# Optimization experiments

Measured on AMD Instinct MI355X. Metric: run time of the kernel, lower is better.

## Reference

```python
import jax, jax.numpy as jnp
import numpy as np

B, N, F_IN, HID, HEADS, LAYERS = 512, 128, 128, 64, 4, 3
NEG_SLOPE = 0.2  # DenseGATConv default


def setup_inputs() -> dict:
    key = jax.random.key(0)
    ks = jax.random.split(key, 1 + 4 * LAYERS)
    inp = {}
    inp["x"] = jax.random.normal(ks[0], (B * N, F_IN), jnp.float32)
    # uniform graph sizes: graph i owns nodes [i*N, (i+1)*N)
    inp["batch_mask"] = jnp.repeat(jnp.arange(B, dtype=jnp.int32), N)
    dims = [F_IN] + [HID * HEADS] * (LAYERS - 1)
    for l in range(LAYERS):
        d = dims[l]
        k = 4 * l
        inp[f"W{l}"] = jax.random.normal(ks[1 + k], (d, HEADS * HID), jnp.float32) / np.sqrt(d)
        inp[f"att_src{l}"] = jax.random.normal(ks[2 + k], (HEADS, HID), jnp.float32) * 0.1
        inp[f"att_dst{l}"] = jax.random.normal(ks[3 + k], (HEADS, HID), jnp.float32) * 0.1
        inp[f"b{l}"] = jnp.zeros((HEADS * HID,), jnp.float32)  # zero-init bias, as in PyG
    return inp


def _dense_gat(x, adj, W, att_src, att_dst, bias):
    # x: [B, N, F_in], adj: [N, N] (shared structure, broadcast over batch)
    b, n, _ = x.shape
    h = (x @ W).reshape(b, n, HEADS, HID)                       # [B,N,H,C]
    a_src = jnp.einsum('bnhc,hc->bnh', h, att_src)              # [B,N,H]
    a_dst = jnp.einsum('bnhc,hc->bnh', h, att_dst)              # [B,N,H]
    # alpha[b,i,j,h] = a_src[b,j,h] + a_dst[b,i,h]
    alpha = a_src[:, None, :, :] + a_dst[:, :, None, :]         # [B,N,N,H]
    alpha = jnp.where(alpha >= 0, alpha, NEG_SLOPE * alpha)
    alpha = jnp.where(adj[None, :, :, None] == 0, -jnp.inf, alpha)
    alpha = jax.nn.softmax(alpha, axis=2)                       # softmax over sources j
    out = jnp.einsum('bijh,bjhc->bihc', alpha, h)               # [B,N,H,C]
    return out.reshape(b, n, HEADS * HID) + bias                # concat heads + bias


def reference(x, batch_mask, W0, att_src0, att_dst0, b0,
              W1, att_src1, att_dst1, b1, W2, att_src2, att_dst2, b2):
    # to_dense_batch with uniform graph sizes == reshape; batch_mask encodes this layout
    h = x.reshape(B, N, F_IN)
    eye = jnp.eye(N, dtype=x.dtype)
    # GNNBlock builds full adjacency with zeroed diagonal ...
    adj = jnp.ones((N, N), x.dtype) - eye
    # ... and DenseGATConv(add_loop=True) re-adds self-loops
    adj = jnp.maximum(adj, eye)
    params = [(W0, att_src0, att_dst0, b0), (W1, att_src1, att_dst1, b1),
              (W2, att_src2, att_dst2, b2)]
    for (W, a_s, a_d, b) in params:
        h = _dense_gat(h, adj, W, a_s, a_d, b)
        # block act is nn.LeakyReLU(True): negative_slope=True==1.0 -> identity
        h = jnp.where(h >= 0, h, 1.0 * h)
    return h.sum(axis=1)  # [B, HEADS*HID]
```

## Files before the change

kernel.cpp:

```cpp
#include <hip/hip_runtime.h>
#include <hip/hip_bf16.h>


typedef unsigned short u16;
typedef __attribute__((ext_vector_type(8))) short short8;
typedef __attribute__((ext_vector_type(4))) float f32x4;

#define L2E 1.44269504088896340736f

__device__ __forceinline__ u16 f2bf(float f) {
  unsigned int u = __float_as_uint(f);
  u += 0x7fffu + ((u >> 16) & 1u);
  return (u16)(u >> 16);
}
__device__ __forceinline__ unsigned int pk2(float a, float b) {
  __hip_bfloat162 h2 = __float22bfloat162_rn(make_float2(a, b));
  unsigned int u;
  __builtin_memcpy(&u, &h2, 4);
  return u;
}

__device__ __forceinline__ int xs_byte(int row, int col) {
  return (row << 9) + ((col << 1) ^ ((row & 7) << 4));
}
__device__ __forceinline__ int ht_byte(int row, int col) {
  return (row << 8) + ((col << 1) ^ ((row & 7) << 4));
}

__global__ void prep_w(const float* __restrict__ W0, const float* __restrict__ W1,
                       const float* __restrict__ W2,
                       const float* __restrict__ as0, const float* __restrict__ ad0,
                       const float* __restrict__ as1, const float* __restrict__ ad1,
                       const float* __restrict__ as2, const float* __restrict__ ad2,
                       u16* __restrict__ wt) {
  const int bid = blockIdx.x, tid = threadIdx.x;
  if (bid < 80) {
    const float* W; int NKB, base, rel;
    if (bid < 16)      { W = W0; NKB = 4; base = 0;      rel = bid; }
    else if (bid < 48) { W = W1; NKB = 8; base = 34816;  rel = bid - 16; }
    else               { W = W2; NKB = 8; base = 104448; rel = bid - 48; }
    const int kb = rel >> 2, ko = rel & 3;
    const int n = tid;
    union { u16 v[8]; short8 s; } u;
    #pragma unroll
    for (int e = 0; e < 8; ++e)
      u.v[e] = f2bf(W[(kb * 32 + ko * 8 + e) * 256 + n]);
    const int t = n >> 4, l15 = n & 15;
    *(short8*)(wt + base + (((t * NKB + kb) * 64 + l15 + (ko << 4)) << 3)) = u.s;
  } else if (bid < 100) {
    int b2 = bid - 80;
    const float* W; const float* as; const float* ad; int NKB, base, kb;
    if (b2 < 4)       { W = W0; as = as0; ad = ad0; NKB = 4; base = 0;      kb = b2; }
    else if (b2 < 12) { W = W1; as = as1; ad = ad1; NKB = 8; base = 34816;  kb = b2 - 4; }
    else              { W = W2; as = as2; ad = ad2; NKB = 8; base = 104448; kb = b2 - 12; }
    const int kloc = tid >> 3, col = tid & 7, h = col & 3;
    const int k = kb * 32 + kloc;
    const float* av = (col < 4) ? as : ad;
    float acc = 0.f;
    #pragma unroll 8
    for (int c = 0; c < 64; ++c)
      acc = fmaf(W[k * 256 + h * 64 + c], av[h * 64 + c], acc);
    const int lane2 = col + ((kloc >> 3) << 4), e = kloc & 7;
    const int tb = base + ((16 * NKB + kb) << 9);
    wt[tb + ((lane2) << 3) + e]     = f2bf(acc);
    wt[tb + ((lane2 + 8) << 3) + e] = 0;
  }
}

__global__ __launch_bounds__(512, 4) void gat_all(
    const float* __restrict__ x, const u16* __restrict__ wt,
    const float* __restrict__ bb0, const float* __restrict__ bb1,
    const float* __restrict__ bb2, float* __restrict__ out)
{
  constexpr int AB = 0;
  constexpr int SB = 65536;
  constexpr int DB = 67584;
  constexpr int PM = 69632;
  constexpr int BS = 69696;
  constexpr int OA = 70720;
  __shared__ __align__(16) unsigned char smem[71744];

  float* sbuf  = (float*)(smem + SB);
  float* dbuf  = (float*)(smem + DB);
  float* pmaxw = (float*)(smem + PM);
  float* bsb   = (float*)(smem + BS);
  float* oac   = (float*)(smem + OA);

  const int b    = blockIdx.x;
  const int tid  = threadIdx.x;
  const int w    = tid >> 6;
  const int lane = tid & 63;
  const int l15  = lane & 15;
  const int lg   = lane >> 4;

  {
    const float4* xg = (const float4*)(x + (size_t)b * (128 * 128));
    #pragma unroll
    for (int it = 0; it < 8; ++it) {
      int e = tid + it * 512;
      float4 v = xg[e];
      int row = e >> 5, c = (e & 31) << 2;
      uint2 u = { pk2(v.x, v.y), pk2(v.z, v.w) };
      *(uint2*)(smem + AB + xs_byte(row, c)) = u;
    }
  }
  __syncthreads();

  const u16* wfl[3]    = {wt, wt + 34816, wt + 104448};
  const float* bias[3] = {bb0, bb1, bb2};

  #pragma unroll
  for (int l = 0; l < 3; ++l) {
    const int NKB = (l == 0) ? 4 : 8;
    const u16* wf = wfl[l];

    if (tid < 256) {
      bsb[tid] = bias[l][tid];
      if (l == 2) oac[tid] = 0.f;
    }

    const int mw = w & 1, nw = w >> 1;
    f32x4 acc[4][4] = {};
    for (int ks = 0; ks < NKB; ++ks) {
      const int kcol = ks * 32 + lg * 8;
      short8 afr[4];
      #pragma unroll
      for (int mi = 0; mi < 4; ++mi)
        afr[mi] = *(const short8*)(smem + AB + xs_byte(mw * 64 + mi * 16 + l15, kcol));
      #pragma unroll
      for (int nh = 0; nh < 2; ++nh) {
        short8 bfr[2];
        #pragma unroll
        for (int ni2 = 0; ni2 < 2; ++ni2) {
          int t = nw * 4 + nh * 2 + ni2;
          bfr[ni2] = *(const short8*)(wf + (((t * NKB + ks) * 64 + lane) << 3));
        }
        #pragma unroll
        for (int mi = 0; mi < 4; ++mi)
          #pragma unroll
          for (int ni2 = 0; ni2 < 2; ++ni2)
            acc[mi][nh * 2 + ni2] = __builtin_amdgcn_mfma_f32_16x16x32_bf16(
                afr[mi], bfr[ni2], acc[mi][nh * 2 + ni2], 0, 0, 0);
      }
    }

    if (w >= 4) {
      const int mw2 = w & 1, mih = (w >> 1) & 1;
      f32x4 acc2[2] = {};
      for (int ks = 0; ks < NKB; ++ks) {
        const int kcol = ks * 32 + lg * 8;
        short8 bsd = *(const short8*)(wf + (((16 * NKB + ks) * 64 + lane) << 3));
        #pragma unroll
        for (int mi2 = 0; mi2 < 2; ++mi2) {
          short8 a = *(const short8*)(smem + AB +
              xs_byte(mw2 * 64 + (mih * 2 + mi2) * 16 + l15, kcol));
          acc2[mi2] = __builtin_amdgcn_mfma_f32_16x16x32_bf16(a, bsd, acc2[mi2], 0, 0, 0);
        }
      }
      float mx = -3.4e38f;
      #pragma unroll
      for (int mi2 = 0; mi2 < 2; ++mi2) {
        f32x4 v = acc2[mi2] * L2E;
        if (l15 < 8) {
          float* basep = (float*)(smem + (l15 < 4 ? SB : DB))
                       + (l15 & 3) * 128 + mw2 * 64 + (mih * 2 + mi2) * 16 + lg * 4;
          *(float4*)basep = (float4){v[0], v[1], v[2], v[3]};
        }
        mx = fmaxf(mx, fmaxf(fmaxf(v[0], v[1]), fmaxf(v[2], v[3])));
      }
      mx = fmaxf(mx, __shfl_xor(mx, 16));
      mx = fmaxf(mx, __shfl_xor(mx, 32));
      if (lane < 4) pmaxw[lane * 4 + (w - 4)] = mx;
    }
    __syncthreads();

    #pragma unroll
    for (int mi = 0; mi < 4; ++mi) {
      int j0 = mw * 64 + mi * 16 + lg * 4;
      #pragma unroll
      for (int ni = 0; ni < 4; ++ni) {
        int c = nw * 64 + ni * 16 + l15;
        uint2 u = { pk2(acc[mi][ni][0], acc[mi][ni][1]),
                    pk2(acc[mi][ni][2], acc[mi][ni][3]) };
        *(uint2*)(smem + AB + ht_byte(c, j0)) = u;
      }
    }
    __syncthreads();

    {
      const int hw = w >> 1, ih = w & 1;
      f32x4 facc[4][4] = {};
      float den[4] = {0.f, 0.f, 0.f, 0.f};
      float dvv[4], nml[4];
      const float smax = fmaxf(fmaxf(pmaxw[hw * 4], pmaxw[hw * 4 + 1]),
                               fmaxf(pmaxw[hw * 4 + 2], pmaxw[hw * 4 + 3]));
      #pragma unroll
      for (int ni = 0; ni < 4; ++ni) {
        int i = ih * 64 + ni * 16 + l15;
        dvv[ni] = dbuf[hw * 128 + i];
        float tm = smax + dvv[ni];
        nml[ni] = -fmaxf(tm, 0.2f * tm);
      }
      #pragma unroll
      for (int ks = 0; ks < 4; ++ks) {
        const int j0 = ks * 32 + lg * 8;
        float4 s03 = *(const float4*)(sbuf + hw * 128 + j0);
        float4 s47 = *(const float4*)(sbuf + hw * 128 + j0 + 4);
        float sj[8] = {s03.x, s03.y, s03.z, s03.w, s47.x, s47.y, s47.z, s47.w};
        short8 afr[4];
        #pragma unroll
        for (int mi = 0; mi < 4; ++mi)
          afr[mi] = *(const short8*)(smem + AB + ht_byte(hw * 64 + mi * 16 + l15, j0));
        #pragma unroll
        for (int ni = 0; ni < 4; ++ni) {
          union { short8 s; unsigned int u[4]; } pk;
          float dsum = 0.f;
          #pragma unroll
          for (int t2 = 0; t2 < 4; ++t2) {
            float ta = sj[2 * t2] + dvv[ni];
            ta = fmaxf(ta, 0.2f * ta);
            float ea = exp2f(ta + nml[ni]);
            float tb = sj[2 * t2 + 1] + dvv[ni];
            tb = fmaxf(tb, 0.2f * tb);
            float eb = exp2f(tb + nml[ni]);
            dsum += ea + eb;
            pk.u[t2] = pk2(ea, eb);
          }
          den[ni] += dsum;
          #pragma unroll
          for (int mi = 0; mi < 4; ++mi)
            facc[mi][ni] = __builtin_amdgcn_mfma_f32_16x16x32_bf16(
                afr[mi], pk.s, facc[mi][ni], 0, 0, 0);
        }
      }
      float rvv[4];
      #pragma unroll
      for (int ni = 0; ni < 4; ++ni) {
        float d2 = den[ni];
        d2 += __shfl_xor(d2, 16);
        d2 += __shfl_xor(d2, 32);
        rvv[ni] = 1.f / d2;
      }
      __syncthreads();

      if (l < 2) {
        #pragma unroll
        for (int mi = 0; mi < 4; ++mi) {
          int c0 = hw * 64 + mi * 16 + lg * 4;
          float b0v = bsb[c0], b1v = bsb[c0 + 1], b2v = bsb[c0 + 2], b3v = bsb[c0 + 3];
          #pragma unroll
          for (int ni = 0; ni < 4; ++ni) {
            int i = ih * 64 + ni * 16 + l15;
            float r = rvv[ni];
            uint2 u = { pk2(fmaf(facc[mi][ni][0], r, b0v), fmaf(facc[mi][ni][1], r, b1v)),
                        pk2(fmaf(facc[mi][ni][2], r, b2v), fmaf(facc[mi][ni][3], r, b3v)) };
            *(uint2*)(smem + AB + xs_byte(i, c0)) = u;
          }
        }
      } else {
        #pragma unroll
        for (int mi = 0; mi < 4; ++mi) {
          #pragma unroll
          for (int reg = 0; reg < 4; ++reg) {
            float pv2 = facc[mi][0][reg] * rvv[0] + facc[mi][1][reg] * rvv[1]
                      + facc[mi][2][reg] * rvv[2] + facc[mi][3][reg] * rvv[3];
            pv2 += __shfl_xor(pv2, 1);
            pv2 += __shfl_xor(pv2, 2);
            pv2 += __shfl_xor(pv2, 4);
            pv2 += __shfl_xor(pv2, 8);
            if (l15 == 0)
              atomicAdd(&oac[hw * 64 + mi * 16 + lg * 4 + reg], pv2);
          }
        }
      }
    }
    __syncthreads();
  }

  if (tid < 256) out[(size_t)b * 256 + tid] = oac[tid] + 128.f * bsb[tid];
}

extern "C" void kernel_launch(void* const* d_in, const int* in_sizes, int n_in,
                              void* d_out, int out_size, void* d_ws, size_t ws_size,
                              hipStream_t stream) {
  const float* x   = (const float*)d_in[0];
  const float* W0  = (const float*)d_in[2];
  const float* as0 = (const float*)d_in[3];
  const float* ad0 = (const float*)d_in[4];
  const float* b0  = (const float*)d_in[5];
  const float* W1  = (const float*)d_in[6];
  const float* as1 = (const float*)d_in[7];
  const float* ad1 = (const float*)d_in[8];
  const float* b1  = (const float*)d_in[9];
  const float* W2  = (const float*)d_in[10];
  const float* as2 = (const float*)d_in[11];
  const float* ad2 = (const float*)d_in[12];
  const float* b2  = (const float*)d_in[13];
  u16* wt = (u16*)d_ws;

  hipLaunchKernelGGL(prep_w, dim3(100), dim3(256), 0, stream,
                     W0, W1, W2, as0, ad0, as1, ad1, as2, ad2, wt);
  hipLaunchKernelGGL(gat_all, dim3(512), dim3(512), 0, stream,
                     x, wt, b0, b1, b2, (float*)d_out);
}
```

Before: 186.5 us.

## Split projection and aggregation into two passes with packed bf16 register staging

The feature projection GEMM and the attention aggregation now each run in two column or row halves. Results are packed to bf16 in registers right after each half, which lowers the peak live fp32 accumulator count. The attention-score GEMM is spread over all 8 waves instead of 4, so the per-wave max reduction buffer grows to 8 entries. The aim is to reduce register pressure and possibly spills under the 512x4 launch bounds, and to balance score work across waves. The cost is that A fragments are reloaded twice and the softmax row loop runs in two passes.

```diff
diff --git a/kernel.cpp b/kernel.cpp
--- a/kernel.cpp
+++ b/kernel.cpp
@@ -76,9 +76,9 @@
   constexpr int SB = 65536;
   constexpr int DB = 67584;
   constexpr int PM = 69632;
-  constexpr int BS = 69696;
-  constexpr int OA = 70720;
-  __shared__ __align__(16) unsigned char smem[71744];
+  constexpr int BS = 69760;
+  constexpr int OA = 70784;
+  __shared__ __align__(16) unsigned char smem[71808];
 
   float* sbuf  = (float*)(smem + SB);
   float* dbuf  = (float*)(smem + DB);
@@ -120,158 +120,172 @@
     }
 
     const int mw = w & 1, nw = w >> 1;
-    f32x4 acc[4][4] = {};
-    for (int ks = 0; ks < NKB; ++ks) {
-      const int kcol = ks * 32 + lg * 8;
-      short8 afr[4];
+    uint2 hpk[2][4][2];
+    #pragma unroll
+    for (int p = 0; p < 2; ++p) {
+      f32x4 acc[4][2] = {};
+      for (int ks = 0; ks < NKB; ++ks) {
+        const int kcol = ks * 32 + lg * 8;
+        short8 afr[4];
+        #pragma unroll
+        for (int mi = 0; mi < 4; ++mi)
+          afr[mi] = *(const short8*)(smem + AB + xs_byte(mw * 64 + mi * 16 + l15, kcol));
+        short8 bfr[2];
+        #pragma unroll
+        for (int ni2 = 0; ni2 < 2; ++ni2) {
+          int t = p * 8 + nw * 2 + ni2;
+          bfr[ni2] = *(const short8*)(wf + (((t * NKB + ks) * 64 + lane) << 3));
+        }
+        #pragma unroll
+        for (int mi = 0; mi < 4; ++mi)
+          #pragma unroll
+          for (int ni2 = 0; ni2 < 2; ++ni2)
+            acc[mi][ni2] = __builtin_amdgcn_mfma_f32_16x16x32_bf16(
+                afr[mi], bfr[ni2], acc[mi][ni2], 0, 0, 0);
+      }
       #pragma unroll
       for (int mi = 0; mi < 4; ++mi)
-        afr[mi] = *(const short8*)(smem + AB + xs_byte(mw * 64 + mi * 16 + l15, kcol));
-      #pragma unroll
-      for (int nh = 0; nh < 2; ++nh) {
-        short8 bfr[2];
-        #pragma unroll
-        for (int ni2 = 0; ni2 < 2; ++ni2) {
-          int t = nw * 4 + nh * 2 + ni2;
-          bfr[ni2] = *(const short8*)(wf + (((t * NKB + ks) * 64 + lane) << 3));
-        }
-        #pragma unroll
-        for (int mi = 0; mi < 4; ++mi)
-          #pragma unroll
-          for (int ni2 = 0; ni2 < 2; ++ni2)
-            acc[mi][nh * 2 + ni2] = __builtin_amdgcn_mfma_f32_16x16x32_bf16(
-                afr[mi], bfr[ni2], acc[mi][nh * 2 + ni2], 0, 0, 0);
-      }
-    }
-
-    if (w >= 4) {
-      const int mw2 = w & 1, mih = (w >> 1) & 1;
-      f32x4 acc2[2] = {};
+        #pragma unroll
+        for (int ni2 = 0; ni2 < 2; ++ni2)
+          hpk[p][mi][ni2] = (uint2){ pk2(acc[mi][ni2][0], acc[mi][ni2][1]),
+                                     pk2(acc[mi][ni2][2], acc[mi][ni2][3]) };
+    }
+
+    {
+      f32x4 acc2 = {};
       for (int ks = 0; ks < NKB; ++ks) {
         const int kcol = ks * 32 + lg * 8;
         short8 bsd = *(const short8*)(wf + (((16 * NKB + ks) * 64 + lane) << 3));
-        #pragma unroll
-        for (int mi2 = 0; mi2 < 2; ++mi2) {
-          short8 a = *(const short8*)(smem + AB +
-              xs_byte(mw2 * 64 + (mih * 2 + mi2) * 16 + l15, kcol));
-          acc2[mi2] = __builtin_amdgcn_mfma_f32_16x16x32_bf16(a, bsd, acc2[mi2], 0, 0, 0);
-        }
-      }
-      float mx = -3.4e38f;
-      #pragma unroll
-      for (int mi2 = 0; mi2 < 2; ++mi2) {
-        f32x4 v = acc2[mi2] * L2E;
-        if (l15 < 8) {
-          float* basep = (float*)(smem + (l15 < 4 ? SB : DB))
-                       + (l15 & 3) * 128 + mw2 * 64 + (mih * 2 + mi2) * 16 + lg * 4;
-          *(float4*)basep = (float4){v[0], v[1], v[2], v[3]};
-        }
-        mx = fmaxf(mx, fmaxf(fmaxf(v[0], v[1]), fmaxf(v[2], v[3])));
-      }
+        short8 a = *(const short8*)(smem + AB + xs_byte(w * 16 + l15, kcol));
+        acc2 = __builtin_amdgcn_mfma_f32_16x16x32_bf16(a, bsd, acc2, 0, 0, 0);
+      }
+      f32x4 v = acc2 * L2E;
+      if (l15 < 8) {
+        float* basep = (float*)(smem + (l15 < 4 ? SB : DB))
+                     + (l15 & 3) * 128 + w * 16 + lg * 4;
+        *(float4*)basep = (float4){v[0], v[1], v[2], v[3]};
+      }
+      float mx = fmaxf(fmaxf(v[0], v[1]), fmaxf(v[2], v[3]));
       mx = fmaxf(mx, __shfl_xor(mx, 16));
       mx = fmaxf(mx, __shfl_xor(mx, 32));
-      if (lane < 4) pmaxw[lane * 4 + (w - 4)] = mx;
+      if (lane < 4) pmaxw[lane * 8 + w] = mx;
     }
     __syncthreads();
 
     #pragma unroll
-    for (int mi = 0; mi < 4; ++mi) {
-      int j0 = mw * 64 + mi * 16 + lg * 4;
+    for (int p = 0; p < 2; ++p)
       #pragma unroll
-      for (int ni = 0; ni < 4; ++ni) {
-        int c = nw * 64 + ni * 16 + l15;
-        uint2 u = { pk2(acc[mi][ni][0], acc[mi][ni][1]),
-                    pk2(acc[mi][ni][2], acc[mi][ni][3]) };
-        *(uint2*)(smem + AB + ht_byte(c, j0)) = u;
-      }
-    }
+      for (int mi = 0; mi < 4; ++mi) {
+        int j0 = mw * 64 + mi * 16 + lg * 4;
+        #pragma unroll
+        for (int ni2 = 0; ni2 < 2; ++ni2) {
+          int c = p * 128 + nw * 32 + ni2 * 16 + l15;
+          *(uint2*)(smem + AB + ht_byte(c, j0)) = hpk[p][mi][ni2];
+        }
+      }
     __syncthreads();
 
     {
       const int hw = w >> 1, ih = w & 1;
-      f32x4 facc[4][4] = {};
-      float den[4] = {0.f, 0.f, 0.f, 0.f};
-      float dvv[4], nml[4];
-      const float smax = fmaxf(fmaxf(pmaxw[hw * 4], pmaxw[hw * 4 + 1]),
-                               fmaxf(pmaxw[hw * 4 + 2], pmaxw[hw * 4 + 3]));
+      float smax = pmaxw[hw * 8];
       #pragma unroll
-      for (int ni = 0; ni < 4; ++ni) {
-        int i = ih * 64 + ni * 16 + l15;
-        dvv[ni] = dbuf[hw * 128 + i];
-        float tm = smax + dvv[ni];
-        nml[ni] = -fmaxf(tm, 0.2f * tm);
-      }
+      for (int q2 = 1; q2 < 8; ++q2) smax = fmaxf(smax, pmaxw[hw * 8 + q2]);
+      uint2 opk[2][4][2];
       #pragma unroll
-      for (int ks = 0; ks < 4; ++ks) {
-        const int j0 = ks * 32 + lg * 8;
-        float4 s03 = *(const float4*)(sbuf + hw * 128 + j0);
-        float4 s47 = *(const float4*)(sbuf + hw * 128 + j0 + 4);
-        float sj[8] = {s03.x, s03.y, s03.z, s03.w, s47.x, s47.y, s47.z, s47.w};
-        short8 afr[4];
-        #pragma unroll
-        for (int mi = 0; mi < 4; ++mi)
-          afr[mi] = *(const short8*)(smem + AB + ht_byte(hw * 64 + mi * 16 + l15, j0));
-        #pragma unroll
-        for (int ni = 0; ni < 4; ++ni) {
-          union { short8 s; unsigned int u[4]; } pk;
-          float dsum = 0.f;
-          #pragma unroll
-          for (int t2 = 0; t2 < 4; ++t2) {
-            float ta = sj[2 * t2] + dvv[ni];
-            ta = fmaxf(ta, 0.2f * ta);
-            float ea = exp2f(ta + nml[ni]);
-            float tb = sj[2 * t2 + 1] + dvv[ni];
-            tb = fmaxf(tb, 0.2f * tb);
-            float eb = exp2f(tb + nml[ni]);
-            dsum += ea + eb;
-            pk.u[t2] = pk2(ea, eb);
+      for (int p = 0; p < 2; ++p) {
+        f32x4 facc[4][2] = {};
+        float den[2] = {0.f, 0.f};
+        float dvv[2], nml[2];
+        #pragma unroll
+        for (int ni = 0; ni < 2; ++ni) {
+          int i = ih * 64 + p * 32 + ni * 16 + l15;
+          dvv[ni] = dbuf[hw * 128 + i];
+          float tm = smax + dvv[ni];
+          nml[ni] = -fmaxf(tm, 0.2f * tm);
+        }
+        #pragma unroll
+        for (int ks = 0; ks < 4; ++ks) {
+          const int j0 = ks * 32 + lg * 8;
+          float4 s03 = *(const float4*)(sbuf + hw * 128 + j0);
+          float4 s47 = *(const float4*)(sbuf + hw * 128 + j0 + 4);
+          float sj[8] = {s03.x, s03.y, s03.z, s03.w, s47.x, s47.y, s47.z, s47.w};
+          short8 afr[4];
+          #pragma unroll
+          for (int mi = 0; mi < 4; ++mi)
+            afr[mi] = *(const short8*)(smem + AB + ht_byte(hw * 64 + mi * 16 + l15, j0));
+          #pragma unroll
+          for (int ni = 0; ni < 2; ++ni) {
+            union { short8 s; unsigned int u[4]; } pk;
+            float dsum = 0.f;
+            #pragma unroll
+            for (int t2 = 0; t2 < 4; ++t2) {
+              float ta = sj[2 * t2] + dvv[ni];
+              ta = fmaxf(ta, 0.2f * ta);
+              float ea = exp2f(ta + nml[ni]);
+              float tb = sj[2 * t2 + 1] + dvv[ni];
+              tb = fmaxf(tb, 0.2f * tb);
+              float eb = exp2f(tb + nml[ni]);
+              dsum += ea + eb;
+              pk.u[t2] = pk2(ea, eb);
+            }
+            den[ni] += dsum;
+            #pragma unroll
+            for (int mi = 0; mi < 4; ++mi)
+              facc[mi][ni] = __builtin_amdgcn_mfma_f32_16x16x32_bf16(
+                  afr[mi], pk.s, facc[mi][ni], 0, 0, 0);
           }
-          den[ni] += dsum;
-          #pragma unroll
-          for (int mi = 0; mi < 4; ++mi)
-            facc[mi][ni] = __builtin_amdgcn_mfma_f32_16x16x32_bf16(
-                afr[mi], pk.s, facc[mi][ni], 0, 0, 0);
-        }
-      }
-      float rvv[4];
-      #pragma unroll
-      for (int ni = 0; ni < 4; ++ni) {
-        float d2 = den[ni];
-        d2 += __shfl_xor(d2, 16);
-        d2 += __shfl_xor(d2, 32);
-        rvv[ni] = 1.f / d2;
+        }
+        float rvv[2];
+        #pragma unroll
+        for (int ni = 0; ni < 2; ++ni) {
+          float d2 = den[ni];
+          d2 += __shfl_xor(d2, 16);
+          d2 += __shfl_xor(d2, 32);
+          rvv[ni] = 1.f / d2;
+        }
+        if (l < 2) {
+          #pragma unroll
+          for (int mi = 0; mi < 4; ++mi) {
+            int c0 = hw * 64 + mi * 16 + lg * 4;
+            float b0v = bsb[c0], b1v = bsb[c0 + 1], b2v = bsb[c0 + 2], b3v = bsb[c0 + 3];
+            #pragma unroll
+            for (int ni = 0; ni < 2; ++ni) {
+              float r = rvv[ni];
+              opk[p][mi][ni] = (uint2){
+                  pk2(fmaf(facc[mi][ni][0], r, b0v), fmaf(facc[mi][ni][1], r, b1v)),
+                  pk2(fmaf(facc[mi][ni][2], r, b2v), fmaf(facc[mi][ni][3], r, b3v)) };
+            }
+          }
+        } else {
+          #pragma unroll
+          for (int mi = 0; mi < 4; ++mi) {
+            #pragma unroll
+            for (int reg = 0; reg < 4; ++reg) {
+              float pv2 = facc[mi][0][reg] * rvv[0] + facc[mi][1][reg] * rvv[1];
+              pv2 += __shfl_xor(pv2, 1);
+              pv2 += __shfl_xor(pv2, 2);
+              pv2 += __shfl_xor(pv2, 4);
+              pv2 += __shfl_xor(pv2, 8);
+              if (l15 == 0)
+                atomicAdd(&oac[hw * 64 + mi * 16 + lg * 4 + reg], pv2);
+            }
+          }
+        }
       }
       __syncthreads();
 
       if (l < 2) {
         #pragma unroll
-        for (int mi = 0; mi < 4; ++mi) {
-          int c0 = hw * 64 + mi * 16 + lg * 4;
-          float b0v = bsb[c0], b1v = bsb[c0 + 1], b2v = bsb[c0 + 2], b3v = bsb[c0 + 3];
-          #pragma unroll
-          for (int ni = 0; ni < 4; ++ni) {
-            int i = ih * 64 + ni * 16 + l15;
-            float r = rvv[ni];
-            uint2 u = { pk2(fmaf(facc[mi][ni][0], r, b0v), fmaf(facc[mi][ni][1], r, b1v)),
-                        pk2(fmaf(facc[mi][ni][2], r, b2v), fmaf(facc[mi][ni][3], r, b3v)) };
-            *(uint2*)(smem + AB + xs_byte(i, c0)) = u;
+        for (int p = 0; p < 2; ++p)
+          #pragma unroll
+          for (int mi = 0; mi < 4; ++mi) {
+            int c0 = hw * 64 + mi * 16 + lg * 4;
+            #pragma unroll
+            for (int ni = 0; ni < 2; ++ni) {
+              int i = ih * 64 + p * 32 + ni * 16 + l15;
+              *(uint2*)(smem + AB + xs_byte(i, c0)) = opk[p][mi][ni];
+            }
           }
-        }
-      } else {
-        #pragma unroll
-        for (int mi = 0; mi < 4; ++mi) {
-          #pragma unroll
-          for (int reg = 0; reg < 4; ++reg) {
-            float pv2 = facc[mi][0][reg] * rvv[0] + facc[mi][1][reg] * rvv[1]
-                      + facc[mi][2][reg] * rvv[2] + facc[mi][3][reg] * rvv[3];
-            pv2 += __shfl_xor(pv2, 1);
-            pv2 += __shfl_xor(pv2, 2);
-            pv2 += __shfl_xor(pv2, 4);
-            pv2 += __shfl_xor(pv2, 8);
-            if (l15 == 0)
-              atomicAdd(&oac[hw * 64 + mi * 16 + lg * 4 + reg], pv2);
-          }
-        }
       }
     }
     __syncthreads();
```

After: 223.4 us. 19.8% more time.
